# Optimization experiments

Measured on AMD Instinct MI355X. Metric: run time of the kernel, lower is better.

## Reference

```python
import jax, jax.numpy as jnp
import numpy as np

E, D, H, T = 8, 1024, 4096, 8192  # num_expert, d_model, d_hidden, total_tokens


def setup_inputs() -> dict:
    key = jax.random.key(0)
    k1, k2, k3, k4, k5 = jax.random.split(key, 5)
    inp = jax.random.normal(k1, (T, D), dtype=jnp.float32)
    # FMoELinear weights: [E, out_features, in_features], bias [E, out_features]
    w1 = jax.random.normal(k2, (E, H, D), dtype=jnp.float32) * 0.02
    b1 = jax.random.normal(k3, (E, H), dtype=jnp.float32) * 0.02
    w2 = jax.random.normal(k4, (E, D, H), dtype=jnp.float32) * 0.02
    b2 = jax.random.normal(k5, (E, D), dtype=jnp.float32) * 0.02
    # tokens are contiguous per expert; equal split here (counts may vary in general)
    fwd_expert_count = jnp.full((E,), T // E, dtype=jnp.int32)
    return {"inp": inp, "w1": w1, "b1": b1, "w2": w2, "b2": b2,
            "fwd_expert_count": fwd_expert_count}


def _expert_ids(counts, n_tokens):
    # token t belongs to expert e iff cumsum(counts)[e-1] <= t < cumsum(counts)[e]
    offsets = jnp.cumsum(counts)  # [E]
    t = jnp.arange(n_tokens)
    return jnp.sum(t[:, None] >= offsets[None, :], axis=1)  # [T] in [0, E]


def _grouped_linear(x, W, b, eid):
    # grouped GEMM: y[t] = W[eid[t]] @ x[t] + b[eid[t]]; tokens with eid >= E -> 0
    n_exp = W.shape[0]
    acc = jnp.zeros((x.shape[0], W.shape[1]), dtype=x.dtype)
    for e in range(n_exp):  # small fixed loop over experts
        ye = x @ W[e].T + b[e]
        acc = acc + jnp.where((eid == e)[:, None], ye, jnp.zeros((), x.dtype))
    return acc


def reference(inp, w1, b1, w2, b2, fwd_expert_count):
    eid = _expert_ids(fwd_expert_count, inp.shape[0])
    h = _grouped_linear(inp, w1, b1, eid)   # [T, H]
    h = jax.nn.gelu(h)
    out = _grouped_linear(h, w2, b2, eid)   # [T, D]
    return out
```

## Files before the change

kernel.cpp:

```cpp
#include <hip/hip_runtime.h>
#include <hip/hip_bf16.h>
#include <cstdint>
#include <cstddef>


using bf16 = __hip_bfloat16;
typedef __attribute__((ext_vector_type(8))) short bf16x8;
typedef __attribute__((ext_vector_type(4))) float f32x4;

#define BM 256
#define BN 256
#define BK 64

typedef const __attribute__((address_space(1))) unsigned int g_u32;
typedef __attribute__((address_space(3))) unsigned int l_u32;

__device__ __forceinline__ void async16(void* lds, const void* g) {
  __builtin_amdgcn_global_load_lds((g_u32*)g, (l_u32*)lds, 16, 0, 0);
}

__device__ __forceinline__ float gelu_f(float x) {
  const float c0 = 0.7978845608028654f;
  const float c1 = 0.044715f;
  float u = c0 * (x + c1 * x * x * x);
  float t = 1.0f - 2.0f / (__expf(2.0f * u) + 1.0f);
  return 0.5f * x * (1.0f + t);
}

__device__ __forceinline__ void cvt8(const float* in, bf16* out, size_t i) {
  f32x4 lo = *(const f32x4*)(in + i);
  f32x4 hi = *(const f32x4*)(in + i + 4);
  bf16 cv[8];
#pragma unroll
  for (int k = 0; k < 4; ++k) {
    cv[k]     = __float2bfloat16(lo[k]);
    cv[k + 4] = __float2bfloat16(hi[k]);
  }
  *(bf16x8*)(out + i) = *(const bf16x8*)cv;
}

__device__ __forceinline__ void bias_fill(float* out, const float* b2,
    const int* counts, int E, int T, int D) {
  for (int row = blockIdx.x; row < T; row += gridDim.x) {
    int eid = 0;
    long long cum = 0;
    for (int e = 0; e < E; ++e) { cum += counts[e]; if (row >= cum) eid = e + 1; }
    f32x4* dst = (f32x4*)(out + (size_t)row * D);
    if (eid < E) {
      const f32x4* src = (const f32x4*)(b2 + (size_t)eid * D);
      for (int c = threadIdx.x; c < (D >> 2); c += blockDim.x) dst[c] = src[c];
    } else {
      const f32x4 z = {};
      for (int c = threadIdx.x; c < (D >> 2); c += blockDim.x) dst[c] = z;
    }
  }
}

__global__ __launch_bounds__(256) void f32_to_bf16_3(
    const float* __restrict__ a, bf16* __restrict__ oa, size_t na,
    const float* __restrict__ b, bf16* __restrict__ ob, size_t nb,
    const float* __restrict__ c, bf16* __restrict__ oc, size_t nc,
    float* out, const float* b2, const int* counts, int E, int T, int D) {
  const size_t stride = (size_t)gridDim.x * blockDim.x * 8;
  const size_t base = ((size_t)blockIdx.x * blockDim.x + threadIdx.x) * 8;
  for (size_t i = base; i < na; i += stride) cvt8(a, oa, i);
  for (size_t i = base; i < nb; i += stride) cvt8(b, ob, i);
  for (size_t i = base; i < nc; i += stride) cvt8(c, oc, i);
  if (out) bias_fill(out, b2, counts, E, T, D);
}

__global__ __launch_bounds__(256) void f32_to_bf16_2(
    const float* __restrict__ a, bf16* __restrict__ oa, size_t na,
    const float* __restrict__ b, bf16* __restrict__ ob, size_t nb,
    float* out, const float* b2, const int* counts, int E, int T, int D) {
  const size_t stride = (size_t)gridDim.x * blockDim.x * 8;
  const size_t base = ((size_t)blockIdx.x * blockDim.x + threadIdx.x) * 8;
  for (size_t i = base; i < na; i += stride) cvt8(a, oa, i);
  if (b) for (size_t i = base; i < nb; i += stride) cvt8(b, ob, i);
  if (out) bias_fill(out, b2, counts, E, T, D);
}

__global__ __launch_bounds__(512) void gemm8p(
    const bf16* __restrict__ A,
    const bf16* __restrict__ B,
    const float* __restrict__ bias,
    void* __restrict__ Cv,
    const int* __restrict__ counts,
    int E, int N, int K, int mode)
{
  __shared__ alignas(16) bf16 As[2][BM * BK];
  __shared__ alignas(16) bf16 Bs[2][BN * BK];

  const int tid  = threadIdx.x;
  const int lane = tid & 63;
  const int wave = tid >> 6;
  const int wm = wave >> 2;
  const int wn = wave & 3;

  const int gx   = gridDim.x;
  const int nwg  = gx * gridDim.y;
  const int orig = blockIdx.y * gx + blockIdx.x;
  const int qq = nwg >> 3, rr = nwg & 7;
  const int xcd = orig & 7, lo = orig >> 3;
  const int wgid = (xcd < rr ? xcd * (qq + 1) : rr * (qq + 1) + (xcd - rr) * qq) + lo;
  const int m0 = (wgid / gx) * BM;
  const int n0 = (wgid % gx) * BN;

  const int klen = K / (int)gridDim.z;
  const int k0 = blockIdx.z * klen;

  int eid = 0;
  {
    long long cum = 0;
    for (int e = 0; e < E; ++e) { cum += counts[e]; if (m0 >= cum) eid = e + 1; }
  }

  f32x4 acc[8][4] = {};

  if (eid < E) {
    const bf16* Ag = A + (size_t)m0 * K;
    const bf16* Bg = B + (size_t)eid * (size_t)N * (size_t)K + (size_t)n0 * K;

    const int swzcol = ((tid & 7) ^ ((tid >> 3) & 7)) * 8;

    const int sk0 = (((lane >> 4) + 0) ^ (lane & 7)) * 16;
    const int sk1 = (((lane >> 4) + 4) ^ (lane & 7)) * 16;
    const int aBase = (wm * 128 + (lane & 15)) * 128;
    const int bBase = (wn * 64  + (lane & 15)) * 128;

    const int nt = klen / BK;

    bf16x8 av[4][2], blo[2][2], bhi[2][2];

#define RD_A(BUF, MI)                                                        \
  { const char* _p = (const char*)&As[BUF][0] + aBase + (MI) * 8192;         \
    _Pragma("unroll") for (int ii = 0; ii < 4; ++ii) {                       \
      av[ii][0] = *(const bf16x8*)(_p + ii * 2048 + sk0);                    \
      av[ii][1] = *(const bf16x8*)(_p + ii * 2048 + sk1); } }

#define RD_B(BUF, HALF, BV)                                                  \
  { const char* _p = (const char*)&Bs[BUF][0] + bBase + (HALF) * 4096;       \
    _Pragma("unroll") for (int jj = 0; jj < 2; ++jj) {                       \
      BV[jj][0] = *(const bf16x8*)(_p + jj * 2048 + sk0);                    \
      BV[jj][1] = *(const bf16x8*)(_p + jj * 2048 + sk1); } }

#define MMAQ(MI, HALF, BV)                                                   \
  _Pragma("unroll") for (int ii = 0; ii < 4; ++ii)                           \
  _Pragma("unroll") for (int jj = 0; jj < 2; ++jj)                           \
  _Pragma("unroll") for (int ks = 0; ks < 2; ++ks)                           \
    acc[(MI)*4 + ii][(HALF)*2 + jj] = __builtin_amdgcn_mfma_f32_16x16x32_bf16( \
      av[ii][ks], BV[jj][ks], acc[(MI)*4 + ii][(HALF)*2 + jj], 0, 0, 0);

#define ST_A(BUF, H, TI)                                                     \
  { const int _kt = k0 + ((TI) < nt ? (TI) : nt - 1) * BK;                   \
    _Pragma("unroll") for (int c = 0; c < 2; ++c) {                          \
      const int _r = (H) * 64 + c * 128 + (tid >> 3);                        \
      async16((char*)&As[BUF][0] + _r * 128 + (tid & 7) * 16,                \
              Ag + (size_t)_r * K + _kt + swzcol); } }

#define ST_B(BUF, H, TI)                                                     \
  { const int _kt = k0 + ((TI) < nt ? (TI) : nt - 1) * BK;                   \
    _Pragma("unroll") for (int c = 0; c < 2; ++c) {                          \
      const int _u = c * 512 + tid;                                          \
      const int _r = (H) * 32 + (_u >> 8) * 64 + ((_u >> 3) & 31);           \
      async16((char*)&Bs[BUF][0] + _r * 128 + (tid & 7) * 16,                \
              Bg + (size_t)_r * K + _kt + swzcol); } }

#define BAR __builtin_amdgcn_s_barrier()
#define VMC6 asm volatile("s_waitcnt vmcnt(6)" ::: "memory")
#define PRIO1 __builtin_amdgcn_s_setprio(1)
#define PRIO0 __builtin_amdgcn_s_setprio(0)

    ST_A(0, 0, 0); ST_B(0, 0, 0); ST_A(0, 1, 0); ST_B(0, 1, 0);
    ST_A(1, 0, 1); ST_B(1, 0, 1); ST_A(1, 1, 1);
    VMC6; BAR;

    for (int it = 0; it < nt / 2; ++it) {
      const int a = 2 * it, b = a + 1;
      RD_A(0, 0); RD_B(0, 0, blo); ST_B(1, 1, b);
      BAR; PRIO1; MMAQ(0, 0, blo); PRIO0; BAR;
      RD_B(0, 1, bhi); ST_A(0, 0, a + 2);
      BAR; PRIO1; MMAQ(0, 1, bhi); PRIO0; BAR;
      RD_A(0, 1); ST_B(0, 0, a + 2);
      BAR; PRIO1; MMAQ(1, 1, bhi); PRIO0; BAR;
      ST_A(0, 1, a + 2); VMC6;
      BAR; PRIO1; MMAQ(1, 0, blo); PRIO0; BAR;
      RD_A(1, 0); RD_B(1, 0, blo); ST_B(0, 1, a + 2);
      BAR; PRIO1; MMAQ(0, 0, blo); PRIO0; BAR;
      RD_B(1, 1, bhi); ST_A(1, 0, b + 2);
      BAR; PRIO1; MMAQ(0, 1, bhi); PRIO0; BAR;
      RD_A(1, 1); ST_B(1, 0, b + 2);
      BAR; PRIO1; MMAQ(1, 1, bhi); PRIO0; BAR;
      ST_A(1, 1, b + 2); VMC6;
      BAR; PRIO1; MMAQ(1, 0, blo); PRIO0; BAR;
    }
    asm volatile("s_waitcnt vmcnt(0)" ::: "memory");

#undef RD_A
#undef RD_B
#undef MMAQ
#undef ST_A
#undef ST_B
#undef BAR
#undef VMC6
#undef PRIO1
#undef PRIO0
  }

  const int crow = (lane >> 4) * 4;
  const int ccol = lane & 15;

  if (eid < E) {
    if (mode == 2) {
      float* outF = (float*)Cv;
#pragma unroll
      for (int i = 0; i < 8; ++i) {
#pragma unroll
        for (int r = 0; r < 4; ++r) {
          const size_t grow = (size_t)(m0 + wm * 128 + i * 16 + crow + r);
#pragma unroll
          for (int j = 0; j < 4; ++j)
            atomicAdd(&outF[grow * N + n0 + wn * 64 + j * 16 + ccol],
                      acc[i][j][r]);
        }
      }
    } else {
      float bv[4];
#pragma unroll
      for (int j = 0; j < 4; ++j)
        bv[j] = bias[(size_t)eid * N + n0 + wn * 64 + j * 16 + ccol];
#pragma unroll
      for (int i = 0; i < 8; ++i) {
#pragma unroll
        for (int r = 0; r < 4; ++r) {
          const size_t grow = (size_t)(m0 + wm * 128 + i * 16 + crow + r);
#pragma unroll
          for (int j = 0; j < 4; ++j) {
            const float v = acc[i][j][r] + bv[j];
            const size_t idx = grow * N + n0 + wn * 64 + j * 16 + ccol;
            if (mode == 1) ((bf16*)Cv)[idx] = __float2bfloat16(gelu_f(v));
            else           ((float*)Cv)[idx] = v;
          }
        }
      }
    }
  } else if (mode != 2) {
#pragma unroll
    for (int i = 0; i < 8; ++i) {
#pragma unroll
      for (int r = 0; r < 4; ++r) {
        const size_t grow = (size_t)(m0 + wm * 128 + i * 16 + crow + r);
#pragma unroll
        for (int j = 0; j < 4; ++j) {
          const size_t idx = grow * N + n0 + wn * 64 + j * 16 + ccol;
          if (mode == 1) ((bf16*)Cv)[idx] = __float2bfloat16(0.0f);
          else           ((float*)Cv)[idx] = 0.0f;
        }
      }
    }
  }
}

#define FBM 128
#define FBK 32

__device__ __forceinline__ void stage_f32(const float* g, bf16* lds,
                                          int srow, int seg, int ldg) {
#pragma unroll
  for (int h = 0; h < 2; ++h) {
    const float* p = g + (size_t)(srow + h * 64) * ldg + seg;
    f32x4 lo = *(const f32x4*)(p);
    f32x4 hi = *(const f32x4*)(p + 4);
    bf16 cv[8];
#pragma unroll
    for (int i = 0; i < 4; ++i) {
      cv[i]     = __float2bfloat16(lo[i]);
      cv[i + 4] = __float2bfloat16(hi[i]);
    }
    *(bf16x8*)&lds[(srow + h * 64) * FBK + seg] = *(const bf16x8*)cv;
  }
}

__device__ __forceinline__ void stage_bf16f(const bf16* g, bf16* lds,
                                            int srow, int seg, int ldg) {
#pragma unroll
  for (int h = 0; h < 2; ++h) {
    const bf16* p = g + (size_t)(srow + h * 64) * ldg + seg;
    *(bf16x8*)&lds[(srow + h * 64) * FBK + seg] = *(const bf16x8*)p;
  }
}

template <bool AF32>
__global__ __launch_bounds__(256) void grouped_gemm_bt(
    const void* __restrict__ Av, const float* __restrict__ B,
    const float* __restrict__ bias, void* __restrict__ Cv,
    const int* __restrict__ counts, int E, int N, int K, int c_is_bf16_gelu)
{
  __shared__ alignas(16) bf16 As[FBM * FBK];
  __shared__ alignas(16) bf16 Bs[FBM * FBK];

  const int tid  = threadIdx.x;
  const int lane = tid & 63;
  const int wave = tid >> 6;
  const int m0 = blockIdx.y * FBM;
  const int n0 = blockIdx.x * FBM;

  int eid = 0;
  {
    long long cum = 0;
    for (int e = 0; e < E; ++e) { cum += counts[e]; if (m0 >= cum) eid = e + 1; }
  }

  const int wrow = (wave >> 1) * 64;
  const int wcol = (wave & 1) * 64;

  f32x4 acc[4][4] = {};

  if (eid < E) {
    const float* Bexp = B + (size_t)eid * (size_t)N * (size_t)K;
    const int srow = tid >> 2;
    const int seg  = (tid & 3) * 8;
    const int frow = lane & 15;
    const int fk   = (lane >> 4) * 8;

    for (int kt = 0; kt < K; kt += FBK) {
      if (AF32)
        stage_f32((const float*)Av + (size_t)(m0 + srow) * K + kt - (size_t)srow * K,
                  As, srow, seg, K);
      else
        stage_bf16f((const bf16*)Av + (size_t)(m0 + srow) * K + kt - (size_t)srow * K,
                    As, srow, seg, K);
      stage_f32(Bexp + (size_t)(n0 + srow) * K + kt - (size_t)srow * K,
                Bs, srow, seg, K);
      __syncthreads();

      bf16x8 af[4], bfr[4];
#pragma unroll
      for (int i = 0; i < 4; ++i)
        af[i] = *(const bf16x8*)&As[(wrow + i * 16 + frow) * FBK + fk];
#pragma unroll
      for (int j = 0; j < 4; ++j)
        bfr[j] = *(const bf16x8*)&Bs[(wcol + j * 16 + frow) * FBK + fk];

#pragma unroll
      for (int i = 0; i < 4; ++i)
#pragma unroll
        for (int j = 0; j < 4; ++j)
          acc[i][j] = __builtin_amdgcn_mfma_f32_16x16x32_bf16(af[i], bfr[j], acc[i][j], 0, 0, 0);

      __syncthreads();
    }
  }

  const int crow = (lane >> 4) * 4;
  const int ccol = lane & 15;
  const int do_gelu = c_is_bf16_gelu;

  if (eid < E) {
    float bv[4];
#pragma unroll
    for (int j = 0; j < 4; ++j)
      bv[j] = bias[(size_t)eid * N + n0 + wcol + j * 16 + ccol];
#pragma unroll
    for (int i = 0; i < 4; ++i) {
#pragma unroll
      for (int r = 0; r < 4; ++r) {
        size_t grow = (size_t)(m0 + wrow + i * 16 + crow + r);
#pragma unroll
        for (int j = 0; j < 4; ++j) {
          float v = acc[i][j][r] + bv[j];
          size_t idx = grow * N + n0 + wcol + j * 16 + ccol;
          if (do_gelu) ((bf16*)Cv)[idx] = __float2bfloat16(gelu_f(v));
          else         ((float*)Cv)[idx] = v;
        }
      }
    }
  } else {
#pragma unroll
    for (int i = 0; i < 4; ++i) {
#pragma unroll
      for (int r = 0; r < 4; ++r) {
        size_t grow = (size_t)(m0 + wrow + i * 16 + crow + r);
#pragma unroll
        for (int j = 0; j < 4; ++j) {
          size_t idx = grow * N + n0 + wcol + j * 16 + ccol;
          if (do_gelu) ((bf16*)Cv)[idx] = __float2bfloat16(0.0f);
          else         ((float*)Cv)[idx] = 0.0f;
        }
      }
    }
  }
}

extern "C" void kernel_launch(void* const* d_in, const int* in_sizes, int n_in,
                              void* d_out, int out_size, void* d_ws, size_t ws_size,
                              hipStream_t stream) {
  const float* inp = (const float*)d_in[0];
  const float* w1  = (const float*)d_in[1];
  const float* b1  = (const float*)d_in[2];
  const float* w2  = (const float*)d_in[3];
  const float* b2  = (const float*)d_in[4];
  const int* cnt   = (const int*)d_in[5];
  float* out = (float*)d_out;

  const int E = in_sizes[5];
  const int H = in_sizes[2] / E;
  const int D = in_sizes[4] / E;
  const int T = in_sizes[0] / D;

  const size_t szH = (size_t)T * H * sizeof(bf16);
  const size_t szX = (size_t)T * D * sizeof(bf16);
  const size_t szW = (size_t)E * (size_t)H * D * sizeof(bf16);

  const size_t nX = (size_t)T * D;
  const size_t nW = (size_t)E * (size_t)H * D;

  const int SPLITK = 2;
  const bool ok8p = (T % BM == 0) && (H % BN == 0) && (D % BN == 0) &&
                    (D % (2 * BK) == 0) && (H % (SPLITK * 2 * BK) == 0);

  dim3 cblk(256), gblk(512);
  dim3 g1(H / BN, T / BM, 1);
  dim3 g2(D / BN, T / BM, SPLITK);

  if (ok8p && ws_size >= szH + szX + 2 * szW) {
    bf16* h   = (bf16*)d_ws;
    bf16* xb  = (bf16*)((char*)d_ws + szH);
    bf16* w1b = (bf16*)((char*)d_ws + szH + szX);
    bf16* w2b = (bf16*)((char*)d_ws + szH + szX + szW);

    f32_to_bf16_3<<<dim3(4096), cblk, 0, stream>>>(
        inp, xb, nX, w1, w1b, nW, w2, w2b, nW, out, b2, cnt, E, T, D);
    gemm8p<<<g1, gblk, 0, stream>>>(xb, w1b, b1, h, cnt, E, H, D, 1);
    gemm8p<<<g2, gblk, 0, stream>>>(h, w2b, b2, out, cnt, E, D, H, 2);
  } else if (ok8p && ws_size >= szH + szX + szW) {
    bf16* h  = (bf16*)d_ws;
    bf16* xb = (bf16*)((char*)d_ws + szH);
    bf16* wb = (bf16*)((char*)d_ws + szH + szX);

    f32_to_bf16_2<<<dim3(2048), cblk, 0, stream>>>(
        inp, xb, nX, w1, wb, nW, out, b2, cnt, E, T, D);
    gemm8p<<<g1, gblk, 0, stream>>>(xb, wb, b1, h, cnt, E, H, D, 1);
    f32_to_bf16_2<<<dim3(2048), cblk, 0, stream>>>(
        w2, wb, nW, nullptr, nullptr, 0, nullptr, nullptr, nullptr, 0, 0, 0);
    gemm8p<<<g2, gblk, 0, stream>>>(h, wb, b2, out, cnt, E, D, H, 2);
  } else {
    bf16* h = (bf16*)d_ws;
    grouped_gemm_bt<true><<<dim3(H / FBM, T / FBM), cblk, 0, stream>>>(
        inp, w1, b1, h, cnt, E, H, D, 1);
    grouped_gemm_bt<false><<<dim3(D / FBM, T / FBM), cblk, 0, stream>>>(
        h, w2, b2, out, cnt, E, D, H, 0);
  }
}
```

Before: 550.0 us.

## Fuse w2 conversion and bias fill into first GEMM epilogue; add LDS waits

Measured after the change: 545.8 us. About the same (-0.8%).

```diff
diff --git a/kernel.cpp b/kernel.cpp
--- a/kernel.cpp
+++ b/kernel.cpp
@@ -39,45 +39,53 @@
   *(bf16x8*)(out + i) = *(const bf16x8*)cv;
 }
 
-__device__ __forceinline__ void bias_fill(float* out, const float* b2,
-    const int* counts, int E, int T, int D) {
-  for (int row = blockIdx.x; row < T; row += gridDim.x) {
+__device__ __forceinline__ void cvt8u2(const float* in, bf16* out, size_t n,
+                                       size_t base, size_t stride) {
+  size_t i = base;
+  for (; i + stride < n; i += 2 * stride) {
+    f32x4 l0 = *(const f32x4*)(in + i);
+    f32x4 h0 = *(const f32x4*)(in + i + 4);
+    f32x4 l1 = *(const f32x4*)(in + i + stride);
+    f32x4 h1 = *(const f32x4*)(in + i + stride + 4);
+    bf16 c0[8], c1[8];
+#pragma unroll
+    for (int k = 0; k < 4; ++k) {
+      c0[k] = __float2bfloat16(l0[k]); c0[k + 4] = __float2bfloat16(h0[k]);
+      c1[k] = __float2bfloat16(l1[k]); c1[k + 4] = __float2bfloat16(h1[k]);
+    }
+    *(bf16x8*)(out + i)          = *(const bf16x8*)c0;
+    *(bf16x8*)(out + i + stride) = *(const bf16x8*)c1;
+  }
+  if (i < n) cvt8(in, out, i);
+}
+
+__device__ __forceinline__ void bias_fill_blk(float* out, const float* b2,
+    const int* counts, int E, int T, int D, int blk, int nblk, int t, int nt) {
+  for (int row = blk; row < T; row += nblk) {
     int eid = 0;
     long long cum = 0;
     for (int e = 0; e < E; ++e) { cum += counts[e]; if (row >= cum) eid = e + 1; }
     f32x4* dst = (f32x4*)(out + (size_t)row * D);
     if (eid < E) {
       const f32x4* src = (const f32x4*)(b2 + (size_t)eid * D);
-      for (int c = threadIdx.x; c < (D >> 2); c += blockDim.x) dst[c] = src[c];
+      for (int c = t; c < (D >> 2); c += nt) dst[c] = src[c];
     } else {
       const f32x4 z = {};
-      for (int c = threadIdx.x; c < (D >> 2); c += blockDim.x) dst[c] = z;
-    }
-  }
-}
-
-__global__ __launch_bounds__(256) void f32_to_bf16_3(
-    const float* __restrict__ a, bf16* __restrict__ oa, size_t na,
-    const float* __restrict__ b, bf16* __restrict__ ob, size_t nb,
-    const float* __restrict__ c, bf16* __restrict__ oc, size_t nc,
-    float* out, const float* b2, const int* counts, int E, int T, int D) {
-  const size_t stride = (size_t)gridDim.x * blockDim.x * 8;
-  const size_t base = ((size_t)blockIdx.x * blockDim.x + threadIdx.x) * 8;
-  for (size_t i = base; i < na; i += stride) cvt8(a, oa, i);
-  for (size_t i = base; i < nb; i += stride) cvt8(b, ob, i);
-  for (size_t i = base; i < nc; i += stride) cvt8(c, oc, i);
-  if (out) bias_fill(out, b2, counts, E, T, D);
-}
-
-__global__ __launch_bounds__(256) void f32_to_bf16_2(
+      for (int c = t; c < (D >> 2); c += nt) dst[c] = z;
+    }
+  }
+}
+
+__global__ __launch_bounds__(256) void cvt_pre(
     const float* __restrict__ a, bf16* __restrict__ oa, size_t na,
     const float* __restrict__ b, bf16* __restrict__ ob, size_t nb,
     float* out, const float* b2, const int* counts, int E, int T, int D) {
   const size_t stride = (size_t)gridDim.x * blockDim.x * 8;
   const size_t base = ((size_t)blockIdx.x * blockDim.x + threadIdx.x) * 8;
-  for (size_t i = base; i < na; i += stride) cvt8(a, oa, i);
-  if (b) for (size_t i = base; i < nb; i += stride) cvt8(b, ob, i);
-  if (out) bias_fill(out, b2, counts, E, T, D);
+  if (a) cvt8u2(a, oa, na, base, stride);
+  if (b) cvt8u2(b, ob, nb, base, stride);
+  if (out) bias_fill_blk(out, b2, counts, E, T, D,
+                         blockIdx.x, gridDim.x, threadIdx.x, blockDim.x);
 }
 
 __global__ __launch_bounds__(512) void gemm8p(
@@ -86,7 +94,9 @@
     const float* __restrict__ bias,
     void* __restrict__ Cv,
     const int* __restrict__ counts,
-    int E, int N, int K, int mode)
+    int E, int N, int K, int mode,
+    const float* __restrict__ sj_src, bf16* __restrict__ sj_dst, size_t sj_n,
+    float* sj_out, const float* sj_b2, int sj_T, int sj_D)
 {
   __shared__ alignas(16) bf16 As[2][BM * BK];
   __shared__ alignas(16) bf16 Bs[2][BN * BK];
@@ -166,6 +176,12 @@
       async16((char*)&Bs[BUF][0] + _r * 128 + (tid & 7) * 16,                \
               Bg + (size_t)_r * K + _kt + swzcol); } }
 
+#define TOPBAR                                                               \
+  __builtin_amdgcn_sched_barrier(0);                                         \
+  __builtin_amdgcn_s_barrier();                                              \
+  asm volatile("s_waitcnt lgkmcnt(0)" ::: "memory");                         \
+  __builtin_amdgcn_sched_barrier(0)
+
 #define BAR __builtin_amdgcn_s_barrier()
 #define VMC6 asm volatile("s_waitcnt vmcnt(6)" ::: "memory")
 #define PRIO1 __builtin_amdgcn_s_setprio(1)
@@ -178,21 +194,21 @@
     for (int it = 0; it < nt / 2; ++it) {
       const int a = 2 * it, b = a + 1;
       RD_A(0, 0); RD_B(0, 0, blo); ST_B(1, 1, b);
-      BAR; PRIO1; MMAQ(0, 0, blo); PRIO0; BAR;
+      TOPBAR; PRIO1; MMAQ(0, 0, blo); PRIO0; BAR;
       RD_B(0, 1, bhi); ST_A(0, 0, a + 2);
-      BAR; PRIO1; MMAQ(0, 1, bhi); PRIO0; BAR;
+      TOPBAR; PRIO1; MMAQ(0, 1, bhi); PRIO0; BAR;
       RD_A(0, 1); ST_B(0, 0, a + 2);
-      BAR; PRIO1; MMAQ(1, 1, bhi); PRIO0; BAR;
+      TOPBAR; PRIO1; MMAQ(1, 1, bhi); PRIO0; BAR;
       ST_A(0, 1, a + 2); VMC6;
-      BAR; PRIO1; MMAQ(1, 0, blo); PRIO0; BAR;
+      TOPBAR; PRIO1; MMAQ(1, 0, blo); PRIO0; BAR;
       RD_A(1, 0); RD_B(1, 0, blo); ST_B(0, 1, a + 2);
-      BAR; PRIO1; MMAQ(0, 0, blo); PRIO0; BAR;
+      TOPBAR; PRIO1; MMAQ(0, 0, blo); PRIO0; BAR;
       RD_B(1, 1, bhi); ST_A(1, 0, b + 2);
-      BAR; PRIO1; MMAQ(0, 1, bhi); PRIO0; BAR;
+      TOPBAR; PRIO1; MMAQ(0, 1, bhi); PRIO0; BAR;
       RD_A(1, 1); ST_B(1, 0, b + 2);
-      BAR; PRIO1; MMAQ(1, 1, bhi); PRIO0; BAR;
+      TOPBAR; PRIO1; MMAQ(1, 1, bhi); PRIO0; BAR;
       ST_A(1, 1, b + 2); VMC6;
-      BAR; PRIO1; MMAQ(1, 0, blo); PRIO0; BAR;
+      TOPBAR; PRIO1; MMAQ(1, 0, blo); PRIO0; BAR;
     }
     asm volatile("s_waitcnt vmcnt(0)" ::: "memory");
 
@@ -201,6 +217,7 @@
 #undef MMAQ
 #undef ST_A
 #undef ST_B
+#undef TOPBAR
 #undef BAR
 #undef VMC6
 #undef PRIO1
@@ -259,6 +276,15 @@
       }
     }
   }
+
+  if (sj_src) {
+    const size_t sstr = (size_t)nwg * blockDim.x * 8;
+    const size_t sbase = ((size_t)orig * blockDim.x + tid) * 8;
+    cvt8u2(sj_src, sj_dst, sj_n, sbase, sstr);
+  }
+  if (sj_out)
+    bias_fill_blk(sj_out, sj_b2, counts, E, sj_T, sj_D,
+                  orig, nwg, tid, blockDim.x);
 }
 
 #define FBM 128
@@ -429,21 +455,25 @@
     bf16* w1b = (bf16*)((char*)d_ws + szH + szX);
     bf16* w2b = (bf16*)((char*)d_ws + szH + szX + szW);
 
-    f32_to_bf16_3<<<dim3(4096), cblk, 0, stream>>>(
-        inp, xb, nX, w1, w1b, nW, w2, w2b, nW, out, b2, cnt, E, T, D);
-    gemm8p<<<g1, gblk, 0, stream>>>(xb, w1b, b1, h, cnt, E, H, D, 1);
-    gemm8p<<<g2, gblk, 0, stream>>>(h, w2b, b2, out, cnt, E, D, H, 2);
+    cvt_pre<<<dim3(2048), cblk, 0, stream>>>(
+        inp, xb, nX, w1, w1b, nW, nullptr, nullptr, nullptr, 0, 0, 0);
+    gemm8p<<<g1, gblk, 0, stream>>>(xb, w1b, b1, h, cnt, E, H, D, 1,
+                                    w2, w2b, nW, out, b2, T, D);
+    gemm8p<<<g2, gblk, 0, stream>>>(h, w2b, b2, out, cnt, E, D, H, 2,
+                                    nullptr, nullptr, 0, nullptr, nullptr, 0, 0);
   } else if (ok8p && ws_size >= szH + szX + szW) {
     bf16* h  = (bf16*)d_ws;
     bf16* xb = (bf16*)((char*)d_ws + szH);
     bf16* wb = (bf16*)((char*)d_ws + szH + szX);
 
-    f32_to_bf16_2<<<dim3(2048), cblk, 0, stream>>>(
+    cvt_pre<<<dim3(2048), cblk, 0, stream>>>(
         inp, xb, nX, w1, wb, nW, out, b2, cnt, E, T, D);
-    gemm8p<<<g1, gblk, 0, stream>>>(xb, wb, b1, h, cnt, E, H, D, 1);
-    f32_to_bf16_2<<<dim3(2048), cblk, 0, stream>>>(
+    gemm8p<<<g1, gblk, 0, stream>>>(xb, wb, b1, h, cnt, E, H, D, 1,
+                                    nullptr, nullptr, 0, nullptr, nullptr, 0, 0);
+    cvt_pre<<<dim3(2048), cblk, 0, stream>>>(
         w2, wb, nW, nullptr, nullptr, 0, nullptr, nullptr, nullptr, 0, 0, 0);
-    gemm8p<<<g2, gblk, 0, stream>>>(h, wb, b2, out, cnt, E, D, H, 2);
+    gemm8p<<<g2, gblk, 0, stream>>>(h, wb, b2, out, cnt, E, D, H, 2,
+                                    nullptr, nullptr, 0, nullptr, nullptr, 0, 0);
   } else {
     bf16* h = (bf16*)d_ws;
     grouped_gemm_bt<true><<<dim3(H / FBM, T / FBM), cblk, 0, stream>>>(
```
